# Optimization experiments

Hardware: AMD Instinct MI355X
Metric: run time of the kernel (lower is better)

Reference implementation:

```python
import jax, jax.numpy as jnp
import numpy as np

# ---- Cl(3,0) Cayley table, basis order [1, e1, e2, e3, e12, e13, e23, e123] ----
def _build_cayley():
    order = [0b000, 0b001, 0b010, 0b100, 0b011, 0b101, 0b110, 0b111]
    idx = {m: i for i, m in enumerate(order)}
    M = np.zeros((8, 8, 8), np.float32)
    for i, a in enumerate(order):
        for j, b in enumerate(order):
            aa, swaps = a >> 1, 0
            while aa:
                swaps += bin(aa & b).count('1')
                aa >>= 1
            M[i, j, idx[a ^ b]] = -1.0 if (swaps % 2) else 1.0
    return M

CAYLEY = jnp.asarray(_build_cayley())  # (8,8,8): c_k = a_i b_j M[i,j,k]

B, D, H, R, K = 16384, 512, 256, 95, 8

def _layernorm(x, g, b, eps=1e-5):
    mu = jnp.mean(x, axis=-1, keepdims=True)
    var = jnp.var(x, axis=-1, keepdims=True)
    return (x - mu) * jax.lax.rsqrt(var + eps) * g + b

def _proj(h, W1, b1, lg, lb, W2, b2):
    x = h @ W1 + b1
    x = _layernorm(x, lg, lb)
    x = jax.nn.gelu(x, approximate=False)  # torch nn.GELU default = exact erf
    return (x @ W2 + b2).reshape(h.shape[0], K, 8)  # dropout is eval-mode identity

def setup_inputs() -> dict:
    key = jax.random.key(0)
    ks = jax.random.split(key, 16)
    s1, s2 = 1.0 / np.sqrt(D), 1.0 / np.sqrt(H)
    inp = {
        'h_perp': jax.random.normal(ks[0], (B, D), jnp.float32),
        'h_vuln': jax.random.normal(ks[1], (B, D), jnp.float32),
        'Wp1': jax.random.normal(ks[2], (D, H), jnp.float32) * s1,
        'bp1': jnp.zeros((H,), jnp.float32),
        'lgp': jnp.ones((H,), jnp.float32),
        'lbp': jnp.zeros((H,), jnp.float32),
        'Wp2': jax.random.normal(ks[3], (H, K * 8), jnp.float32) * s2,
        'bp2': jnp.zeros((K * 8,), jnp.float32),
        'Wv1': jax.random.normal(ks[4], (D, H), jnp.float32) * s1,
        'bv1': jnp.zeros((H,), jnp.float32),
        'lgv': jnp.ones((H,), jnp.float32),
        'lbv': jnp.zeros((H,), jnp.float32),
        'Wv2': jax.random.normal(ks[5], (H, K * 8), jnp.float32) * s2,
        'bv2': jnp.zeros((K * 8,), jnp.float32),
        'T': jax.random.normal(ks[6], (R, K, 8), jnp.float32) * 0.1,
        'gw': jnp.zeros((8,), jnp.float32).at[0].set(1.0),
    }
    return inp

def reference(h_perp, h_vuln, Wp1, bp1, lgp, lbp, Wp2, bp2,
              Wv1, bv1, lgv, lbv, Wv2, bv2, T, gw):
    m_perp = _proj(h_perp, Wp1, bp1, lgp, lbp, Wp2, bp2)  # (B,K,8)
    m_vuln = _proj(h_vuln, Wv1, bv1, lgv, lbv, Wv2, bv2)  # (B,K,8)
    # triple product: (m_perp x T_r) x m_vuln  via Cayley tensor
    at = jnp.einsum('bki,rkj,ijm->brkm', m_perp, T, CAYLEY)          # (B,R,K,8)
    res = jnp.einsum('brkm,bkj,mjn->brkn', at, m_vuln, CAYLEY)       # (B,R,K,8)
    weighted = jnp.einsum('brkn,n->brk', res, gw)                    # grade-weighted readout
    return jnp.mean(weighted, axis=-1)                               # (B,R) logits
```

## Files before the change

kernel.cpp:

```cpp
#include <hip/hip_runtime.h>
#include <math.h>


#define B_ 16384
#define D_ 512
#define H_ 256
#define R_ 95

typedef __attribute__((ext_vector_type(8))) short short8;
typedef __attribute__((ext_vector_type(4))) float f32x4;

#define MFMA(a, b, c) __builtin_amdgcn_mfma_f32_16x16x32_bf16(a, b, c, 0, 0, 0)

__device__ __forceinline__ short f2bf(float x) {
    union { float f; unsigned u; } v; v.f = x;
    unsigned r = v.u + 0x7fffu + ((v.u >> 16) & 1u);
    return (short)(r >> 16);
}
__device__ __forceinline__ float bf2f(short s) {
    union { float f; unsigned u; } v;
    v.u = ((unsigned)(unsigned short)s) << 16;
    return v.f;
}

__device__ __forceinline__ float gelu_fast(float x) {
    const float z  = x * 0.70710678118654752f;
    const float az = fabsf(z);
    const float t  = 1.0f / fmaf(0.3275911f, az, 1.0f);
    float p = fmaf(1.061405429f, t, -1.453152027f);
    p = fmaf(p, t, 1.421413741f);
    p = fmaf(p, t, -0.284496736f);
    p = fmaf(p, t, 0.254829592f);
    p *= t;
    const float e  = 1.0f - p * __expf(-az * az);
    const float er = copysignf(e, z);
    return 0.5f * x * (1.0f + er);
}

__global__ __launch_bounds__(256)
void cdd_prep_kernel(const float* __restrict__ Wp1, const float* __restrict__ Wv1,
                     const float* __restrict__ Wp2, const float* __restrict__ Wv2,
                     short* __restrict__ W1c_p, short* __restrict__ W1c_v,
                     short* __restrict__ W2t_p, short* __restrict__ W2t_v)
{
    const int o = blockIdx.x * 256 + threadIdx.x;
    if (o < 16 * 256 * 32) {
        const int n = o & 255, kin = (o >> 8) & 31, ch = o >> 13;
        const int src = (ch * 32 + kin) * 256 + n;
        const int dst = ch * 8192 + n * 32 + kin;
        W1c_p[dst] = f2bf(Wp1[src]);
        W1c_v[dst] = f2bf(Wv1[src]);
    }
    if (o < 64 * 256) {
        const int n = o >> 8, k = o & 255;
        W2t_p[o] = f2bf(Wp2[k * 64 + n]);
        W2t_v[o] = f2bf(Wv2[k * 64 + n]);
    }
}

__global__ __launch_bounds__(256, 2)
void cdd_proj_kernel(const float* __restrict__ h_p, const float* __restrict__ h_v,
                     const float* __restrict__ bp1, const float* __restrict__ lgp,
                     const float* __restrict__ lbp, const float* __restrict__ bp2,
                     const float* __restrict__ bv1, const float* __restrict__ lgv,
                     const float* __restrict__ lbv, const float* __restrict__ bv2,
                     const short* __restrict__ W1c_p, const short* __restrict__ W1c_v,
                     const short* __restrict__ W2t_p, const short* __restrict__ W2t_v,
                     short* __restrict__ mp_out, short* __restrict__ mv_out)
{
    __shared__ __align__(16) short hs[32 * 40];
    __shared__ __align__(16) short xs[32 * 264];
    __shared__ __align__(16) float lnbuf[256];

    const int which = blockIdx.y;
    const float* __restrict__ h   = which ? h_v : h_p;
    const float* __restrict__ b1  = which ? bv1 : bp1;
    const float* __restrict__ lg  = which ? lgv : lgp;
    const float* __restrict__ lb  = which ? lbv : lbp;
    const float* __restrict__ b2  = which ? bv2 : bp2;
    const short* __restrict__ W1c = which ? W1c_v : W1c_p;
    const short* __restrict__ W2t = which ? W2t_v : W2t_p;
    short* __restrict__ mo = which ? mv_out : mp_out;

    const int t = threadIdx.x;
    const int w = t >> 6, l = t & 63, q = l >> 4, c = l & 15;
    const int b0 = blockIdx.x * 32;
    const int hrow = t >> 3, hk = (t & 7) * 4;

    f32x4 acc1[2][4];
#pragma unroll
    for (int mt = 0; mt < 2; ++mt)
#pragma unroll
        for (int nt = 0; nt < 4; ++nt) acc1[mt][nt] = 0;

    const size_t hoff = (size_t)(b0 + hrow) * D_ + hk;
    const short* Wb0 = W1c + (w * 64 + c) * 32 + q * 8;

    for (int ch = 0; ch < 16; ++ch) {
        const float4 hv = *(const float4*)(h + hoff + ch * 32);
        short8 wb[4];
#pragma unroll
        for (int nt = 0; nt < 4; ++nt)
            wb[nt] = *(const short8*)(Wb0 + ch * 8192 + nt * 512);

        __syncthreads();
        union { short s[4]; uint2 u; } pk;
        pk.s[0] = f2bf(hv.x); pk.s[1] = f2bf(hv.y);
        pk.s[2] = f2bf(hv.z); pk.s[3] = f2bf(hv.w);
        *(uint2*)(hs + hrow * 40 + hk) = pk.u;
        __syncthreads();

        const short8 a0 = *(const short8*)(hs + c * 40 + q * 8);
        const short8 a1 = *(const short8*)(hs + (16 + c) * 40 + q * 8);
#pragma unroll
        for (int nt = 0; nt < 4; ++nt) {
            acc1[0][nt] = MFMA(a0, wb[nt], acc1[0][nt]);
            acc1[1][nt] = MFMA(a1, wb[nt], acc1[1][nt]);
        }
    }

    float bb[4], gg[4], ee[4];
#pragma unroll
    for (int nt = 0; nt < 4; ++nt) {
        const int col = w * 64 + nt * 16 + c;
        bb[nt] = b1[col]; gg[nt] = lg[col]; ee[nt] = lb[col];
    }
    float mean[2][4], rstd[2][4];
#pragma unroll
    for (int mt = 0; mt < 2; ++mt)
#pragma unroll
        for (int reg = 0; reg < 4; ++reg) {
            float s1 = 0.f, s2 = 0.f;
#pragma unroll
            for (int nt = 0; nt < 4; ++nt) {
                const float a = acc1[mt][nt][reg] + bb[nt];
                acc1[mt][nt][reg] = a;
                s1 += a; s2 += a * a;
            }
#pragma unroll
            for (int m = 1; m <= 8; m <<= 1) {
                s1 += __shfl_xor(s1, m, 64);
                s2 += __shfl_xor(s2, m, 64);
            }
            if (c == 0) {
                const int row = mt * 16 + q * 4 + reg;
                *(float2*)(lnbuf + (w * 32 + row) * 2) = make_float2(s1, s2);
            }
        }
    __syncthreads();
#pragma unroll
    for (int mt = 0; mt < 2; ++mt)
#pragma unroll
        for (int reg = 0; reg < 4; ++reg) {
            const int row = mt * 16 + q * 4 + reg;
            float S1 = 0.f, S2 = 0.f;
#pragma unroll
            for (int w2 = 0; w2 < 4; ++w2) {
                const float2 p = *(const float2*)(lnbuf + (w2 * 32 + row) * 2);
                S1 += p.x; S2 += p.y;
            }
            const float mu = S1 * (1.f / 256.f);
            const float var = S2 * (1.f / 256.f) - mu * mu;
            mean[mt][reg] = mu;
            rstd[mt][reg] = rsqrtf(var + 1e-5f);
        }
#pragma unroll
    for (int mt = 0; mt < 2; ++mt)
#pragma unroll
        for (int reg = 0; reg < 4; ++reg) {
            const int row = mt * 16 + q * 4 + reg;
            const float mu = mean[mt][reg], rs = rstd[mt][reg];
#pragma unroll
            for (int nt = 0; nt < 4; ++nt) {
                const int col = w * 64 + nt * 16 + c;
                const float xv = (acc1[mt][nt][reg] - mu) * rs * gg[nt] + ee[nt];
                xs[row * 264 + col] = f2bf(gelu_fast(xv));
            }
        }
    __syncthreads();

    f32x4 acc2[2]; acc2[0] = 0; acc2[1] = 0;
    const short* W2b = W2t + (w * 16 + c) * 256 + q * 8;
#pragma unroll
    for (int ks = 0; ks < 8; ++ks) {
        const short8 xa0 = *(const short8*)(xs + c * 264 + ks * 32 + q * 8);
        const short8 xa1 = *(const short8*)(xs + (16 + c) * 264 + ks * 32 + q * 8);
        const short8 wbk = *(const short8*)(W2b + ks * 32);
        acc2[0] = MFMA(xa0, wbk, acc2[0]);
        acc2[1] = MFMA(xa1, wbk, acc2[1]);
    }
    const float bc = b2[w * 16 + c];
#pragma unroll
    for (int mt = 0; mt < 2; ++mt)
#pragma unroll
        for (int reg = 0; reg < 4; ++reg) {
            const int row = mt * 16 + q * 4 + reg;
            mo[(size_t)(b0 + row) * 64 + w * 16 + c] = f2bf(acc2[mt][reg] + bc);
        }
}

__global__ __launch_bounds__(256, 2)
void cdd_cliff_kernel(const short* __restrict__ mp, const short* __restrict__ mv,
                      const float* __restrict__ T, const float* __restrict__ gw,
                      float* __restrict__ out)
{
    __shared__ __align__(16) float wfl[32 * 68];
    __shared__ __align__(16) float ts[95 * 68];
    const int t  = threadIdx.x;
    const int b0 = blockIdx.x * 32;

#pragma unroll
    for (int k = 0; k < 6; ++k) {
        const int o = t + k * 256;
        if (o < 95 * 16) {
            const int rr = o >> 4, c4 = (o & 15) << 2;
            *(float4*)(ts + rr * 68 + c4) = *(const float4*)(T + rr * 64 + c4);
        }
    }

    {
        const int row = t >> 3, kq = t & 7;
        float g[8];
#pragma unroll
        for (int i = 0; i < 8; ++i) g[i] = gw[i];
        const short8 p8 = *(const short8*)(mp + (size_t)(b0 + row) * 64 + kq * 8);
        const short8 q8 = *(const short8*)(mv + (size_t)(b0 + row) * 64 + kq * 8);
        float mpv[8], mvv[8];
#pragma unroll
        for (int i = 0; i < 8; ++i) { mpv[i] = bf2f(p8[i]); mvv[i] = bf2f(q8[i]); }

        constexpr int MSK[8] = {0, 1, 2, 4, 3, 5, 6, 7};
        float v[8];
#pragma unroll
        for (int m = 0; m < 8; ++m) {
            float s = 0.f;
#pragma unroll
            for (int j = 0; j < 8; ++j) {
                const int am = MSK[m], bm = MSK[j];
                const int par = (__popc((am >> 1) & bm) + __popc((am >> 2) & bm)) & 1;
                const float sg = par ? -1.f : 1.f;
                s = fmaf(sg * g[MSK[am ^ bm]], mvv[j], s);
            }
            v[m] = s;
        }
#pragma unroll
        for (int l2 = 0; l2 < 8; ++l2) {
            float s = 0.f;
#pragma unroll
            for (int i = 0; i < 8; ++i) {
                const int am = MSK[i], bm = MSK[l2];
                const int par = (__popc((am >> 1) & bm) + __popc((am >> 2) & bm)) & 1;
                const float sg = par ? -1.f : 1.f;
                s = fmaf(sg * mpv[i], v[MSK[am ^ bm]], s);
            }
            wfl[row * 68 + kq * 8 + l2] = s;
        }
    }
    __syncthreads();

    {
        const int rr = t >> 3, rl = t & 7;
        float4 wv[16];
#pragma unroll
        for (int cc = 0; cc < 16; ++cc)
            wv[cc] = *(const float4*)(wfl + rr * 68 + cc * 4);
#pragma unroll
        for (int k = 0; k < 12; ++k) {
            const int r = rl + (k << 3);
            if (r < R_) {
                float s = 0.f;
#pragma unroll
                for (int cc = 0; cc < 16; ++cc) {
                    const float4 tv = *(const float4*)(ts + r * 68 + cc * 4);
                    s += wv[cc].x * tv.x + wv[cc].y * tv.y
                       + wv[cc].z * tv.z + wv[cc].w * tv.w;
                }
                out[(size_t)(b0 + rr) * R_ + r] = 0.125f * s;
            }
        }
    }
}

extern "C" void kernel_launch(void* const* d_in, const int* in_sizes, int n_in,
                              void* d_out, int out_size, void* d_ws, size_t ws_size,
                              hipStream_t stream)
{
    const float* h_p = (const float*)d_in[0];
    const float* h_v = (const float*)d_in[1];
    const float* Wp1 = (const float*)d_in[2];
    const float* bp1 = (const float*)d_in[3];
    const float* lgp = (const float*)d_in[4];
    const float* lbp = (const float*)d_in[5];
    const float* Wp2 = (const float*)d_in[6];
    const float* bp2 = (const float*)d_in[7];
    const float* Wv1 = (const float*)d_in[8];
    const float* bv1 = (const float*)d_in[9];
    const float* lgv = (const float*)d_in[10];
    const float* lbv = (const float*)d_in[11];
    const float* Wv2 = (const float*)d_in[12];
    const float* bv2 = (const float*)d_in[13];
    const float* T   = (const float*)d_in[14];
    const float* gw  = (const float*)d_in[15];
    float* out = (float*)d_out;

    short* W1c_p = (short*)d_ws;
    short* W1c_v = W1c_p + 16 * 256 * 32;
    short* W2t_p = W1c_v + 16 * 256 * 32;
    short* W2t_v = W2t_p + 64 * 256;
    short* mp    = W2t_v + 64 * 256;
    short* mv    = mp + (size_t)B_ * 64;

    cdd_prep_kernel<<<512, 256, 0, stream>>>(Wp1, Wv1, Wp2, Wv2,
                                             W1c_p, W1c_v, W2t_p, W2t_v);
    dim3 g1(B_ / 32, 2);
    cdd_proj_kernel<<<g1, 256, 0, stream>>>(h_p, h_v,
                                            bp1, lgp, lbp, bp2,
                                            bv1, lgv, lbv, bv2,
                                            W1c_p, W1c_v, W2t_p, W2t_v,
                                            mp, mv);
    cdd_cliff_kernel<<<B_ / 32, 256, 0, stream>>>(mp, mv, T, gw, out);
}
```

Baseline: 162.6 us.

## Stage full h tile in LDS upfront and double-buffer W1 fragment loads

Loads the entire 32x512 input tile into shared memory once, converting to bf16 in an MFMA-fragment-friendly layout. This removes the two barriers per K-chunk. The K loop is restructured to process chunk pairs, prefetching the next W1 fragments into registers while MFMAs run on the current ones. Shared memory use grows from about 2.5KB to 32KB for the h tile, which may reduce occupancy, and register pressure rises from the double-buffered weights.

```diff
diff --git a/kernel.cpp b/kernel.cpp
--- a/kernel.cpp
+++ b/kernel.cpp
@@ -68,7 +68,7 @@
                      const short* __restrict__ W2t_p, const short* __restrict__ W2t_v,
                      short* __restrict__ mp_out, short* __restrict__ mv_out)
 {
-    __shared__ __align__(16) short hs[32 * 40];
+    __shared__ __align__(16) short hs[32 * 512];
     __shared__ __align__(16) short xs[32 * 264];
     __shared__ __align__(16) float lnbuf[256];
 
@@ -85,7 +85,24 @@
     const int t = threadIdx.x;
     const int w = t >> 6, l = t & 63, q = l >> 4, c = l & 15;
     const int b0 = blockIdx.x * 32;
-    const int hrow = t >> 3, hk = (t & 7) * 4;
+
+    {
+        const int row = t >> 3, kbase = (t & 7) * 64;
+        const int mt_s = row >> 4, c_s = row & 15;
+        const float* hrp = h + (size_t)(b0 + row) * D_ + kbase;
+#pragma unroll
+        for (int s = 0; s < 8; ++s) {
+            const float4 u0 = *(const float4*)(hrp + s * 8);
+            const float4 u1 = *(const float4*)(hrp + s * 8 + 4);
+            short8 pk;
+            pk[0] = f2bf(u0.x); pk[1] = f2bf(u0.y); pk[2] = f2bf(u0.z); pk[3] = f2bf(u0.w);
+            pk[4] = f2bf(u1.x); pk[5] = f2bf(u1.y); pk[6] = f2bf(u1.z); pk[7] = f2bf(u1.w);
+            const int k0 = kbase + s * 8;
+            const int ch = k0 >> 5, qd = (k0 & 31) >> 3;
+            *(short8*)(hs + (ch * 2 + mt_s) * 512 + (qd * 16 + c_s) * 8) = pk;
+        }
+    }
+    __syncthreads();
 
     f32x4 acc1[2][4];
 #pragma unroll
@@ -93,29 +110,39 @@
 #pragma unroll
         for (int nt = 0; nt < 4; ++nt) acc1[mt][nt] = 0;
 
-    const size_t hoff = (size_t)(b0 + hrow) * D_ + hk;
     const short* Wb0 = W1c + (w * 64 + c) * 32 + q * 8;
-
-    for (int ch = 0; ch < 16; ++ch) {
-        const float4 hv = *(const float4*)(h + hoff + ch * 32);
-        short8 wb[4];
+    short8 wb0[4], wb1[4];
+#pragma unroll
+    for (int nt = 0; nt < 4; ++nt) wb0[nt] = *(const short8*)(Wb0 + nt * 512);
+
+#pragma unroll 1
+    for (int cp = 0; cp < 8; ++cp) {
+        const int ch0 = cp * 2, ch1 = cp * 2 + 1;
 #pragma unroll
         for (int nt = 0; nt < 4; ++nt)
-            wb[nt] = *(const short8*)(Wb0 + ch * 8192 + nt * 512);
-
-        __syncthreads();
-        union { short s[4]; uint2 u; } pk;
-        pk.s[0] = f2bf(hv.x); pk.s[1] = f2bf(hv.y);
-        pk.s[2] = f2bf(hv.z); pk.s[3] = f2bf(hv.w);
-        *(uint2*)(hs + hrow * 40 + hk) = pk.u;
-        __syncthreads();
-
-        const short8 a0 = *(const short8*)(hs + c * 40 + q * 8);
-        const short8 a1 = *(const short8*)(hs + (16 + c) * 40 + q * 8);
-#pragma unroll
-        for (int nt = 0; nt < 4; ++nt) {
-            acc1[0][nt] = MFMA(a0, wb[nt], acc1[0][nt]);
-            acc1[1][nt] = MFMA(a1, wb[nt], acc1[1][nt]);
+            wb1[nt] = *(const short8*)(Wb0 + ch1 * 8192 + nt * 512);
+        {
+            const short8 a0 = *(const short8*)(hs + (ch0 * 2 + 0) * 512 + l * 8);
+            const short8 a1 = *(const short8*)(hs + (ch0 * 2 + 1) * 512 + l * 8);
+#pragma unroll
+            for (int nt = 0; nt < 4; ++nt) {
+                acc1[0][nt] = MFMA(a0, wb0[nt], acc1[0][nt]);
+                acc1[1][nt] = MFMA(a1, wb0[nt], acc1[1][nt]);
+            }
+        }
+        if (cp < 7) {
+#pragma unroll
+            for (int nt = 0; nt < 4; ++nt)
+                wb0[nt] = *(const short8*)(Wb0 + (ch0 + 2) * 8192 + nt * 512);
+        }
+        {
+            const short8 a0 = *(const short8*)(hs + (ch1 * 2 + 0) * 512 + l * 8);
+            const short8 a1 = *(const short8*)(hs + (ch1 * 2 + 1) * 512 + l * 8);
+#pragma unroll
+            for (int nt = 0; nt < 4; ++nt) {
+                acc1[0][nt] = MFMA(a0, wb1[nt], acc1[0][nt]);
+                acc1[1][nt] = MFMA(a1, wb1[nt], acc1[1][nt]);
+            }
         }
     }
 
```

Result: no change. 163.8 us (+0.7%).

## Stage h in quarter-K LDS chunks with prefetched loads and double-buffered weights

Applied to the files above, without the earlier changes.

The first GEMM loop now converts and stores 128 columns of h per stage into an MFMA-fragment-ordered LDS layout, cutting barriers from two per 32-wide chunk to about two per 128-wide quarter. Global loads of the next h quarter and the next W1 fragments are issued ahead of use, hiding memory latency behind the MFMAs. The LayerNorm statistics and normalization loops are merged, which drops the mean/rstd arrays. This uses more LDS and registers, which may reduce occupancy.

```diff
diff --git a/kernel.cpp b/kernel.cpp
--- a/kernel.cpp
+++ b/kernel.cpp
@@ -68,7 +68,7 @@
                      const short* __restrict__ W2t_p, const short* __restrict__ W2t_v,
                      short* __restrict__ mp_out, short* __restrict__ mv_out)
 {
-    __shared__ __align__(16) short hs[32 * 40];
+    __shared__ __align__(16) short hs[8 * 512];
     __shared__ __align__(16) short xs[32 * 264];
     __shared__ __align__(16) float lnbuf[256];
 
@@ -85,7 +85,8 @@
     const int t = threadIdx.x;
     const int w = t >> 6, l = t & 63, q = l >> 4, c = l & 15;
     const int b0 = blockIdx.x * 32;
-    const int hrow = t >> 3, hk = (t & 7) * 4;
+    const int srow = t >> 3, kq8 = (t & 7) * 16;
+    const int mt_s = srow >> 4, c_s = srow & 15;
 
     f32x4 acc1[2][4];
 #pragma unroll
@@ -93,29 +94,57 @@
 #pragma unroll
         for (int nt = 0; nt < 4; ++nt) acc1[mt][nt] = 0;
 
-    const size_t hoff = (size_t)(b0 + hrow) * D_ + hk;
     const short* Wb0 = W1c + (w * 64 + c) * 32 + q * 8;
-
-    for (int ch = 0; ch < 16; ++ch) {
-        const float4 hv = *(const float4*)(h + hoff + ch * 32);
-        short8 wb[4];
-#pragma unroll
-        for (int nt = 0; nt < 4; ++nt)
-            wb[nt] = *(const short8*)(Wb0 + ch * 8192 + nt * 512);
-
+    short8 wb0[4], wb1[4];
+#pragma unroll
+    for (int nt = 0; nt < 4; ++nt) wb0[nt] = *(const short8*)(Wb0 + nt * 512);
+
+    const float* hbase = h + (size_t)(b0 + srow) * D_ + kq8;
+    float4 ha[2], hb[2];
+#pragma unroll
+    for (int s = 0; s < 2; ++s) {
+        ha[s] = *(const float4*)(hbase + s * 8);
+        hb[s] = *(const float4*)(hbase + s * 8 + 4);
+    }
+
+    for (int qh = 0; qh < 4; ++qh) {
+        if (qh) __syncthreads();
+#pragma unroll
+        for (int s = 0; s < 2; ++s) {
+            short8 pk;
+            pk[0] = f2bf(ha[s].x); pk[1] = f2bf(ha[s].y);
+            pk[2] = f2bf(ha[s].z); pk[3] = f2bf(ha[s].w);
+            pk[4] = f2bf(hb[s].x); pk[5] = f2bf(hb[s].y);
+            pk[6] = f2bf(hb[s].z); pk[7] = f2bf(hb[s].w);
+            const int kk = kq8 + s * 8;
+            const int chl = kk >> 5, qd = (kk >> 3) & 3;
+            *(short8*)(hs + (chl * 2 + mt_s) * 512 + (qd * 16 + c_s) * 8) = pk;
+        }
+        if (qh < 3) {
+#pragma unroll
+            for (int s = 0; s < 2; ++s) {
+                ha[s] = *(const float4*)(hbase + (qh + 1) * 128 + s * 8);
+                hb[s] = *(const float4*)(hbase + (qh + 1) * 128 + s * 8 + 4);
+            }
+        }
         __syncthreads();
-        union { short s[4]; uint2 u; } pk;
-        pk.s[0] = f2bf(hv.x); pk.s[1] = f2bf(hv.y);
-        pk.s[2] = f2bf(hv.z); pk.s[3] = f2bf(hv.w);
-        *(uint2*)(hs + hrow * 40 + hk) = pk.u;
-        __syncthreads();
-
-        const short8 a0 = *(const short8*)(hs + c * 40 + q * 8);
-        const short8 a1 = *(const short8*)(hs + (16 + c) * 40 + q * 8);
-#pragma unroll
-        for (int nt = 0; nt < 4; ++nt) {
-            acc1[0][nt] = MFMA(a0, wb[nt], acc1[0][nt]);
-            acc1[1][nt] = MFMA(a1, wb[nt], acc1[1][nt]);
+
+        for (int chl = 0; chl < 4; ++chl) {
+            const int g = qh * 4 + chl;
+            if (g < 15) {
+#pragma unroll
+                for (int nt = 0; nt < 4; ++nt)
+                    wb1[nt] = *(const short8*)(Wb0 + (g + 1) * 8192 + nt * 512);
+            }
+            const short8 a0 = *(const short8*)(hs + (chl * 2 + 0) * 512 + l * 8);
+            const short8 a1 = *(const short8*)(hs + (chl * 2 + 1) * 512 + l * 8);
+#pragma unroll
+            for (int nt = 0; nt < 4; ++nt) {
+                acc1[0][nt] = MFMA(a0, wb0[nt], acc1[0][nt]);
+                acc1[1][nt] = MFMA(a1, wb0[nt], acc1[1][nt]);
+            }
+#pragma unroll
+            for (int nt = 0; nt < 4; ++nt) wb0[nt] = wb1[nt];
         }
     }
 
@@ -125,7 +154,6 @@
         const int col = w * 64 + nt * 16 + c;
         bb[nt] = b1[col]; gg[nt] = lg[col]; ee[nt] = lb[col];
     }
-    float mean[2][4], rstd[2][4];
 #pragma unroll
     for (int mt = 0; mt < 2; ++mt)
 #pragma unroll
@@ -159,17 +187,9 @@
                 const float2 p = *(const float2*)(lnbuf + (w2 * 32 + row) * 2);
                 S1 += p.x; S2 += p.y;
             }
-            const float mu = S1 * (1.f / 256.f);
+            const float mu  = S1 * (1.f / 256.f);
             const float var = S2 * (1.f / 256.f) - mu * mu;
-            mean[mt][reg] = mu;
-            rstd[mt][reg] = rsqrtf(var + 1e-5f);
-        }
-#pragma unroll
-    for (int mt = 0; mt < 2; ++mt)
-#pragma unroll
-        for (int reg = 0; reg < 4; ++reg) {
-            const int row = mt * 16 + q * 4 + reg;
-            const float mu = mean[mt][reg], rs = rstd[mt][reg];
+            const float rs  = rsqrtf(var + 1e-5f);
 #pragma unroll
             for (int nt = 0; nt < 4; ++nt) {
                 const int col = w * 64 + nt * 16 + c;
```

After: 158.3 us. 1.03x faster.
